# Kernel optimization log

Measured on AMD Instinct MI355X. Metric: run time of the kernel, lower is better.

Reference implementation:

```python
import jax, jax.numpy as jnp
import numpy as np

DIM = 1024
HEADS = 16
HEAD_DIM = DIM // HEADS
SCALE = HEAD_DIM ** -0.5


def setup_inputs() -> dict:
    key = jax.random.key(0)
    k1, k2, k3, k4 = jax.random.split(key, 4)
    x = jax.random.normal(k1, (8, 1024, DIM), dtype=jnp.float32)
    # qkv: Linear(dim, 3*dim), bias=False; proj: Linear(dim, dim) with bias
    w_qkv = jax.random.normal(k2, (DIM, 3 * DIM), dtype=jnp.float32) * (DIM ** -0.5)
    w_proj = jax.random.normal(k3, (DIM, DIM), dtype=jnp.float32) * (DIM ** -0.5)
    b_proj = jax.random.normal(k4, (DIM,), dtype=jnp.float32) * 0.02
    return {"x": x, "w_qkv": w_qkv, "w_proj": w_proj, "b_proj": b_proj}


def reference(x, w_qkv, w_proj, b_proj):
    b, n, dim = x.shape
    h, d = HEADS, HEAD_DIM
    qkv = x @ w_qkv                                  # [b, n, 3*dim]
    qkv = qkv.reshape(b, n, 3, h, d)                  # split (qkv h d)
    q = jnp.transpose(qkv[:, :, 0], (0, 2, 1, 3))     # [b, h, n, d]
    k = jnp.transpose(qkv[:, :, 1], (0, 2, 1, 3))
    v = jnp.transpose(qkv[:, :, 2], (0, 2, 1, 3))
    dots = jnp.einsum('bhid,bhjd->bhij', q, k) * SCALE
    attn = jax.nn.softmax(dots, axis=-1)              # [b, h, n, n]
    out = jnp.einsum('bhij,bhjd->bhid', attn, v)      # [b, h, n, d]
    out = jnp.transpose(out, (0, 2, 1, 3)).reshape(b, n, dim)
    return out @ w_proj + b_proj
```

## Files before the change

kernel.cpp:

```cpp
#include <hip/hip_runtime.h>
#include <hip/hip_bf16.h>
#include <stdint.h>


typedef __attribute__((ext_vector_type(8))) short  short8;
typedef __attribute__((ext_vector_type(4))) float  floatx4;

#define MFMA_BF16(a, b, c) __builtin_amdgcn_mfma_f32_16x16x32_bf16((a), (b), (c), 0, 0, 0)

__device__ __forceinline__ uint16_t f2b(float f) {
    uint32_t i; __builtin_memcpy(&i, &f, 4);
    uint32_t r = i + 0x7FFFu + ((i >> 16) & 1u);
    return (uint16_t)(r >> 16);
}

#if defined(__has_builtin)
#if __has_builtin(__builtin_amdgcn_cvt_pk_bf16_f32)
#define HAVE_PK_BF16 1
#endif
#if __has_builtin(__builtin_amdgcn_exp2f)
#define EXP2F __builtin_amdgcn_exp2f
#endif
#endif
#ifndef EXP2F
#define EXP2F exp2f
#endif

__device__ __forceinline__ uint32_t pk_bf16(float a, float b) {
#ifdef HAVE_PK_BF16
    typedef __attribute__((ext_vector_type(2))) __bf16 bf16x2;
    bf16x2 v = __builtin_amdgcn_cvt_pk_bf16_f32(a, b);
    uint32_t u; __builtin_memcpy(&u, &v, 4); return u;
#else
    return (uint32_t)f2b(a) | ((uint32_t)f2b(b) << 16);
#endif
}

__device__ __forceinline__ void p32swap(uint32_t& a, uint32_t& b) {
    asm("v_permlane32_swap_b32 %0, %1" : "+v"(a), "+v"(b));
}
__device__ __forceinline__ void p16swap(uint32_t& a, uint32_t& b) {
    asm("v_permlane16_swap_b32 %0, %1" : "+v"(a), "+v"(b));
}

__device__ __forceinline__ void async16(uint16_t* lds, const uint16_t* g) {
    __builtin_amdgcn_global_load_lds(
        (const __attribute__((address_space(1))) uint32_t*)g,
        (__attribute__((address_space(3))) uint32_t*)lds,
        16, 0, 0);
}

__global__ __launch_bounds__(256) void cvt_f32_bf16(
    const float* __restrict__ in, uint16_t* __restrict__ out, int n4)
{
    const int i = blockIdx.x * 256 + threadIdx.x;
    if (i < n4) {
        const float4 v = ((const float4*)in)[i];
        ushort4 o;
        o.x = f2b(v.x); o.y = f2b(v.y); o.z = f2b(v.z); o.w = f2b(v.w);
        ((ushort4*)out)[i] = o;
    }
}

__global__ __launch_bounds__(256) void transpose_k(
    const float* __restrict__ in, uint16_t* __restrict__ out, int R, int C)
{
    __shared__ uint16_t t[32][33];
    const int bx = blockIdx.x * 32;
    const int by = blockIdx.y * 32;
    const int tx = threadIdx.x & 31, ty = threadIdx.x >> 5;
    #pragma unroll
    for (int j = 0; j < 32; j += 8)
        t[ty + j][tx] = f2b(in[(size_t)(by + ty + j) * C + bx + tx]);
    __syncthreads();
    #pragma unroll
    for (int j = 0; j < 32; j += 8)
        out[(size_t)(bx + ty + j) * R + by + tx] = t[tx][ty + j];
}

template <int EPI>
__global__ __launch_bounds__(256, 2) void gemm_bt(
    const uint16_t* __restrict__ A, const uint16_t* __restrict__ Bt,
    uint16_t* __restrict__ C, float* __restrict__ Cf,
    const float* __restrict__ bias, int M, int N, int K)
{
    __shared__ uint16_t As[128 * 64];
    __shared__ uint16_t Bs[128 * 64];

    const int tid  = threadIdx.x;
    const int lane = tid & 63, quad = lane >> 4, l16 = lane & 15;
    const int wv   = tid >> 6;
    const int wm   = (wv >> 1) * 64, wn = (wv & 1) * 64;

    const int lid = blockIdx.y * gridDim.x + blockIdx.x;
    const int nxl = gridDim.x >> 3;
    const int xcd = lid & 7, loc = lid >> 3;
    const int bx  = xcd * nxl + (loc % nxl);
    const int by  = loc / nxl;
    const int tm  = by * 128, tn = bx * 128;

    floatx4 acc[4][4] = {};

    for (int kt = 0; kt < K; kt += 64) {
        __syncthreads();
        #pragma unroll
        for (int i = 0; i < 4; i++) {
            const int li  = i * 256 + tid;
            const int row = li >> 3;
            const int cg  = (li & 7) ^ (row & 7);
            async16(&As[li * 8], &A[(size_t)(tm + row) * K + kt + cg * 8]);
        }
        #pragma unroll
        for (int i = 0; i < 4; i++) {
            const int li  = i * 256 + tid;
            const int row = li >> 3;
            const int cg  = (li & 7) ^ (row & 7);
            async16(&Bs[li * 8], &Bt[(size_t)(tn + row) * K + kt + cg * 8]);
        }
        __syncthreads();
        #pragma unroll
        for (int kc = 0; kc < 2; kc++) {
            short8 af[4], bf[4];
            #pragma unroll
            for (int mb = 0; mb < 4; mb++) {
                const int row = wm + mb * 16 + l16;
                const int g   = kc * 4 + quad;
                af[mb] = *(const short8*)&As[row * 64 + ((g ^ (row & 7)) * 8)];
            }
            #pragma unroll
            for (int nb = 0; nb < 4; nb++) {
                const int row = wn + nb * 16 + l16;
                const int g   = kc * 4 + quad;
                bf[nb] = *(const short8*)&Bs[row * 64 + ((g ^ (row & 7)) * 8)];
            }
            #pragma unroll
            for (int mb = 0; mb < 4; mb++)
                #pragma unroll
                for (int nb = 0; nb < 4; nb++)
                    acc[mb][nb] = MFMA_BF16(af[mb], bf[nb], acc[mb][nb]);
        }
    }

    if (EPI == 0) {
        const int which = (tn + wn) >> 10;
        if (which == 2) {
            #pragma unroll
            for (int nb = 0; nb < 4; nb++) {
                const int col = tn + wn + nb * 16 + l16;
                const int hh = (col >> 6) & 15, dd = col & 63;
                #pragma unroll
                for (int mb = 0; mb < 4; mb++) {
                    const int gm = tm + wm + mb * 16 + quad * 4;
                    const int b  = gm >> 10, n = gm & 1023;
                    const size_t rgn = (size_t)(256 + b * 16 + hh) * 65536;
                    uint2 o;
                    o.x = pk_bf16(acc[mb][nb][0], acc[mb][nb][1]);
                    o.y = pk_bf16(acc[mb][nb][2], acc[mb][nb][3]);
                    *(uint2*)&C[rgn + (size_t)dd * 1024 + n] = o;
                }
            }
        } else {
            const float qs = (which == 0) ? 0.18033688011112043f : 1.0f;
            #pragma unroll
            for (int nb = 0; nb < 4; nb++) {
                const int col = tn + wn + nb * 16 + l16;
                const int hh = (col >> 6) & 15, dd = col & 63;
                #pragma unroll
                for (int mb = 0; mb < 4; mb++)
                    #pragma unroll
                    for (int r = 0; r < 4; r++) {
                        const int gm = tm + wm + mb * 16 + quad * 4 + r;
                        const int b  = gm >> 10, n = gm & 1023;
                        const size_t rgn = (size_t)(which * 128 + b * 16 + hh) * 65536;
                        C[rgn + (size_t)n * 64 + dd] = f2b(acc[mb][nb][r] * qs);
                    }
            }
        }
    } else {
        #pragma unroll
        for (int nb = 0; nb < 4; nb++) {
            const int col = tn + wn + nb * 16 + l16;
            const float bv = bias[col];
            #pragma unroll
            for (int mb = 0; mb < 4; mb++)
                #pragma unroll
                for (int r = 0; r < 4; r++) {
                    const int gm = tm + wm + mb * 16 + quad * 4 + r;
                    Cf[(size_t)gm * N + col] = acc[mb][nb][r] + bv;
                }
        }
    }
}

__global__ __launch_bounds__(256, 4) void attn_fa(
    const uint16_t* __restrict__ qkv, uint16_t* __restrict__ out)
{
    __shared__ uint16_t Ks[128 * 64];
    __shared__ uint16_t Vs[64 * 128];

    const int tid  = threadIdx.x;
    const int lane = tid & 63, quad = lane >> 4, l16 = lane & 15;
    const int wv   = tid >> 6;
    const int bh   = blockIdx.y;
    const int q0   = blockIdx.x * 128 + wv * 32;

    const size_t qbase  = (size_t)bh * 65536;
    const size_t kbase  = (size_t)(128 + bh) * 65536;
    const size_t vtbase = (size_t)(256 + bh) * 65536;

    short8 qf[2][2];
    #pragma unroll
    for (int nq = 0; nq < 2; nq++)
        #pragma unroll
        for (int ks = 0; ks < 2; ks++)
            qf[nq][ks] = *(const short8*)&qkv[qbase + (size_t)(q0 + nq * 16 + l16) * 64 + ks * 32 + quad * 8];

    floatx4 Oacc[2][4] = {};
    float lpart[2] = {0.f, 0.f};

    for (int kb = 0; kb < 8; kb++) {
        __syncthreads();
        #pragma unroll
        for (int i = 0; i < 4; i++) {
            const int li  = i * 256 + tid;
            const int row = li >> 3;
            const int cg  = (li & 7) ^ (row & 7);
            async16(&Ks[li * 8], &qkv[kbase + (size_t)(kb * 128 + row) * 64 + cg * 8]);
        }
        #pragma unroll
        for (int i = 0; i < 4; i++) {
            const int li  = i * 256 + tid;
            const int row = li >> 4;
            const int cg  = (li & 15) ^ (row & 15);
            async16(&Vs[li * 8], &qkv[vtbase + (size_t)row * 1024 + kb * 128 + cg * 8]);
        }
        __syncthreads();

        #pragma unroll
        for (int h = 0; h < 2; h++) {
            short8 pf[2][2];
            #pragma unroll
            for (int kk = 0; kk < 2; kk++) {
                floatx4 st[2][2];
                #pragma unroll
                for (int mb2 = 0; mb2 < 2; mb2++) {
                    const int krow = h * 64 + (kk * 2 + mb2) * 16 + l16;
                    const int g0 = quad, g1 = 4 + quad;
                    short8 kf0 = *(const short8*)&Ks[krow * 64 + ((g0 ^ (krow & 7)) * 8)];
                    short8 kf1 = *(const short8*)&Ks[krow * 64 + ((g1 ^ (krow & 7)) * 8)];
                    #pragma unroll
                    for (int nq = 0; nq < 2; nq++) {
                        floatx4 z = {};
                        z = MFMA_BF16(kf0, qf[nq][0], z);
                        z = MFMA_BF16(kf1, qf[nq][1], z);
                        st[mb2][nq] = z;
                    }
                }
                #pragma unroll
                for (int mb2 = 0; mb2 < 2; mb2++)
                    #pragma unroll
                    for (int nq = 0; nq < 2; nq++)
                        #pragma unroll
                        for (int r = 0; r < 4; r++) {
                            const float p = EXP2F(st[mb2][nq][r]);
                            st[mb2][nq][r] = p;
                            lpart[nq] += p;
                        }
                #pragma unroll
                for (int nq = 0; nq < 2; nq++) {
                    uint32_t w0 = pk_bf16(st[0][nq][0], st[0][nq][1]);
                    uint32_t w1 = pk_bf16(st[0][nq][2], st[0][nq][3]);
                    uint32_t w2 = pk_bf16(st[1][nq][0], st[1][nq][1]);
                    uint32_t w3 = pk_bf16(st[1][nq][2], st[1][nq][3]);
                    p32swap(w0, w2); p16swap(w0, w2);
                    p32swap(w1, w3); p16swap(w1, w3);
                    uint32_t w[4] = { w0, w1, w2, w3 };
                    __builtin_memcpy(&pf[nq][kk], w, 16);
                }
            }
            #pragma unroll
            for (int nb = 0; nb < 4; nb++)
                #pragma unroll
                for (int kk = 0; kk < 2; kk++) {
                    const int vrow = nb * 16 + l16;
                    const int g    = h * 8 + kk * 4 + quad;
                    short8 vf = *(const short8*)&Vs[vrow * 128 + ((g ^ (vrow & 15)) * 8)];
                    #pragma unroll
                    for (int qb = 0; qb < 2; qb++)
                        Oacc[qb][nb] = MFMA_BF16(pf[qb][kk], vf, Oacc[qb][nb]);
                }
        }
    }

    float linv[2];
    #pragma unroll
    for (int nq = 0; nq < 2; nq++) {
        float l = lpart[nq];
        l += __shfl_xor(l, 16);
        l += __shfl_xor(l, 32);
        linv[nq] = 1.f / l;
    }
    float inv[2][4];
    #pragma unroll
    for (int qb = 0; qb < 2; qb++)
        #pragma unroll
        for (int r = 0; r < 4; r++)
            inv[qb][r] = __shfl(linv[qb], quad * 4 + r);

    const int b = bh >> 4, hh = bh & 15;
    #pragma unroll
    for (int qb = 0; qb < 2; qb++)
        #pragma unroll
        for (int nb = 0; nb < 4; nb++)
            #pragma unroll
            for (int r = 0; r < 4; r++) {
                const int n = q0 + qb * 16 + quad * 4 + r;
                out[((size_t)(b * 1024 + n)) * 1024 + hh * 64 + nb * 16 + l16] =
                    f2b(Oacc[qb][nb][r] * inv[qb][r]);
            }
}

extern "C" void kernel_launch(void* const* d_in, const int* in_sizes, int n_in,
                              void* d_out, int out_size, void* d_ws, size_t ws_size,
                              hipStream_t stream)
{
    const float* x      = (const float*)d_in[0];
    const float* w_qkv  = (const float*)d_in[1];
    const float* w_proj = (const float*)d_in[2];
    const float* b_proj = (const float*)d_in[3];
    float* out = (float*)d_out;

    uint16_t* ws   = (uint16_t*)d_ws;
    uint16_t* xb   = ws;
    uint16_t* wTq  = xb  + 8192 * 1024;
    uint16_t* wTp  = wTq + 3072 * 1024;
    uint16_t* qkvb = wTp + 1024 * 1024;
    uint16_t* ao   = xb;

    cvt_f32_bf16<<<8192, 256, 0, stream>>>(x, xb, 8192 * 1024 / 4);
    transpose_k<<<dim3(96, 32), 256, 0, stream>>>(w_qkv, wTq, 1024, 3072);
    transpose_k<<<dim3(32, 32), 256, 0, stream>>>(w_proj, wTp, 1024, 1024);
    gemm_bt<0><<<dim3(24, 64), 256, 0, stream>>>(xb, wTq, qkvb, nullptr, nullptr, 8192, 3072, 1024);
    attn_fa<<<dim3(8, 128), 256, 0, stream>>>(qkvb, ao);
    gemm_bt<1><<<dim3(8, 64), 256, 0, stream>>>(ao, wTp, nullptr, out, b_proj, 8192, 1024, 1024);
}
```

Before: 237.5 us.

## Double-buffer GEMM LDS tiles with 256x128 blocks and split-phase prefetch

Rewrites the bf16 GEMM main loop to use 512-thread blocks covering 256x128 output tiles with double-buffered LDS. Global-to-LDS async loads for the next k-tile are issued in halves between the two MFMA phases, with explicit vmcnt waits, barriers and setprio, so memory traffic overlaps compute instead of stalling at each k-step. This doubles LDS use to about 96KB per block and relies on the epilogue still mapping wm/wn correctly with the larger M tile. Grid sizes are halved in M to match.

New measurement: 245.8 us. 3.5% more time.

```diff
diff --git a/kernel.cpp b/kernel.cpp
--- a/kernel.cpp
+++ b/kernel.cpp
@@ -78,66 +78,120 @@
         out[(size_t)(bx + ty + j) * R + by + tx] = t[tx][ty + j];
 }
 
+__device__ __forceinline__ void stage_a(uint16_t* dst, const uint16_t* src,
+                                        int row0, int K, int kt, int half, int tid)
+{
+    #pragma unroll
+    for (int s = 0; s < 2; s++) {
+        const int li = s * 512 + tid;
+        const int r  = li >> 3;
+        const int R  = ((r >> 5) << 6) + half * 32 + (r & 31);
+        const int cg = (li & 7) ^ (R & 7);
+        async16(&dst[R * 64 + (li & 7) * 8],
+                &src[(size_t)(row0 + R) * K + kt + cg * 8]);
+    }
+}
+__device__ __forceinline__ void stage_b(uint16_t* dst, const uint16_t* src,
+                                        int row0, int K, int kt, int tid)
+{
+    #pragma unroll
+    for (int s = 0; s < 2; s++) {
+        const int li = s * 512 + tid;
+        const int r  = li >> 3;
+        const int cg = (li & 7) ^ (r & 7);
+        async16(&dst[li * 8],
+                &src[(size_t)(row0 + r) * K + kt + cg * 8]);
+    }
+}
+
 template <int EPI>
-__global__ __launch_bounds__(256, 2) void gemm_bt(
+__global__ __launch_bounds__(512, 2) void gemm_bt(
     const uint16_t* __restrict__ A, const uint16_t* __restrict__ Bt,
     uint16_t* __restrict__ C, float* __restrict__ Cf,
     const float* __restrict__ bias, int M, int N, int K)
 {
-    __shared__ uint16_t As[128 * 64];
-    __shared__ uint16_t Bs[128 * 64];
+    __shared__ uint16_t As[2][256 * 64];
+    __shared__ uint16_t Bs[2][128 * 64];
 
     const int tid  = threadIdx.x;
     const int lane = tid & 63, quad = lane >> 4, l16 = lane & 15;
     const int wv   = tid >> 6;
-    const int wm   = (wv >> 1) * 64, wn = (wv & 1) * 64;
+    const int wm   = (wv >> 1) * 64;
+    const int wn   = (wv & 1) * 64;
 
     const int lid = blockIdx.y * gridDim.x + blockIdx.x;
     const int nxl = gridDim.x >> 3;
     const int xcd = lid & 7, loc = lid >> 3;
     const int bx  = xcd * nxl + (loc % nxl);
     const int by  = loc / nxl;
-    const int tm  = by * 128, tn = bx * 128;
+    const int tm  = by * 256, tn = bx * 128;
+
+    const int nt = K >> 6;
 
     floatx4 acc[4][4] = {};
 
-    for (int kt = 0; kt < K; kt += 64) {
-        __syncthreads();
-        #pragma unroll
-        for (int i = 0; i < 4; i++) {
-            const int li  = i * 256 + tid;
-            const int row = li >> 3;
-            const int cg  = (li & 7) ^ (row & 7);
-            async16(&As[li * 8], &A[(size_t)(tm + row) * K + kt + cg * 8]);
-        }
-        #pragma unroll
-        for (int i = 0; i < 4; i++) {
-            const int li  = i * 256 + tid;
-            const int row = li >> 3;
-            const int cg  = (li & 7) ^ (row & 7);
-            async16(&Bs[li * 8], &Bt[(size_t)(tn + row) * K + kt + cg * 8]);
-        }
-        __syncthreads();
-        #pragma unroll
-        for (int kc = 0; kc < 2; kc++) {
-            short8 af[4], bf[4];
-            #pragma unroll
-            for (int mb = 0; mb < 4; mb++) {
-                const int row = wm + mb * 16 + l16;
-                const int g   = kc * 4 + quad;
-                af[mb] = *(const short8*)&As[row * 64 + ((g ^ (row & 7)) * 8)];
+    stage_a(&As[0][0], A,  tm, K, 0,  0, tid);
+    stage_a(&As[0][0], A,  tm, K, 0,  1, tid);
+    stage_b(&Bs[0][0], Bt, tn, K, 0,     tid);
+    stage_a(&As[1][0], A,  tm, K, 64, 0, tid);
+    __builtin_amdgcn_sched_barrier(0);
+    asm volatile("s_waitcnt vmcnt(2)" ::: "memory");
+    __builtin_amdgcn_s_barrier();
+
+    for (int t = 0; t < nt; t++) {
+        const int cur = t & 1;
+        const uint16_t* Ac = &As[cur][0];
+        const uint16_t* Bc = &Bs[cur][0];
+        #pragma unroll
+        for (int p = 0; p < 2; p++) {
+            short8 af[2][2], bfr[4][2];
+            #pragma unroll
+            for (int mb = 0; mb < 2; mb++) {
+                const int row = wm + p * 32 + mb * 16 + l16;
+                #pragma unroll
+                for (int kc = 0; kc < 2; kc++) {
+                    const int g = kc * 4 + quad;
+                    af[mb][kc] = *(const short8*)&Ac[row * 64 + ((g ^ (row & 7)) * 8)];
+                }
             }
             #pragma unroll
             for (int nb = 0; nb < 4; nb++) {
                 const int row = wn + nb * 16 + l16;
-                const int g   = kc * 4 + quad;
-                bf[nb] = *(const short8*)&Bs[row * 64 + ((g ^ (row & 7)) * 8)];
-            }
-            #pragma unroll
-            for (int mb = 0; mb < 4; mb++)
+                #pragma unroll
+                for (int kc = 0; kc < 2; kc++) {
+                    const int g = kc * 4 + quad;
+                    bfr[nb][kc] = *(const short8*)&Bc[row * 64 + ((g ^ (row & 7)) * 8)];
+                }
+            }
+            if (p == 0) {
+                if (t + 1 < nt) {
+                    stage_b(&Bs[cur ^ 1][0], Bt, tn, K, (t + 1) << 6, tid);
+                    stage_a(&As[cur ^ 1][0], A,  tm, K, (t + 1) << 6, 1, tid);
+                }
+            } else {
+                if (t + 2 < nt)
+                    stage_a(&As[cur][0], A, tm, K, (t + 2) << 6, 0, tid);
+            }
+            __builtin_amdgcn_sched_barrier(0);
+            __builtin_amdgcn_s_barrier();
+            asm volatile("" ::: "memory");
+            __builtin_amdgcn_s_setprio(1);
+            #pragma unroll
+            for (int mb = 0; mb < 2; mb++)
                 #pragma unroll
                 for (int nb = 0; nb < 4; nb++)
-                    acc[mb][nb] = MFMA_BF16(af[mb], bf[nb], acc[mb][nb]);
+                    #pragma unroll
+                    for (int kc = 0; kc < 2; kc++)
+                        acc[p * 2 + mb][nb] =
+                            MFMA_BF16(af[mb][kc], bfr[nb][kc], acc[p * 2 + mb][nb]);
+            __builtin_amdgcn_s_setprio(0);
+            __builtin_amdgcn_sched_barrier(0);
+            if (p == 1) {
+                if (t + 2 < nt) { asm volatile("s_waitcnt vmcnt(2)" ::: "memory"); }
+                else            { asm volatile("s_waitcnt vmcnt(0)" ::: "memory"); }
+            }
+            __builtin_amdgcn_s_barrier();
+            __builtin_amdgcn_sched_barrier(0);
         }
     }
 
@@ -340,7 +394,7 @@
     cvt_f32_bf16<<<8192, 256, 0, stream>>>(x, xb, 8192 * 1024 / 4);
     transpose_k<<<dim3(96, 32), 256, 0, stream>>>(w_qkv, wTq, 1024, 3072);
     transpose_k<<<dim3(32, 32), 256, 0, stream>>>(w_proj, wTp, 1024, 1024);
-    gemm_bt<0><<<dim3(24, 64), 256, 0, stream>>>(xb, wTq, qkvb, nullptr, nullptr, 8192, 3072, 1024);
+    gemm_bt<0><<<dim3(24, 32), 512, 0, stream>>>(xb, wTq, qkvb, nullptr, nullptr, 8192, 3072, 1024);
     attn_fa<<<dim3(8, 128), 256, 0, stream>>>(qkvb, ao);
-    gemm_bt<1><<<dim3(8, 64), 256, 0, stream>>>(ao, wTp, nullptr, out, b_proj, 8192, 1024, 1024);
-}
+    gemm_bt<1><<<dim3(8, 32), 512, 0, stream>>>(ao, wTp, nullptr, out, b_proj, 8192, 1024, 1024);
+}
```

## Double-buffer K/V tiles in attention with async prefetch two blocks ahead

Applied to the files above, without the earlier changes.

Replaces the single 128-key K/V shared tile, loaded synchronously each iteration, with two 64-key buffers. The loads for block kb+2 are issued right after block kb is consumed, and manual vmcnt waits plus barriers keep global loads overlapped with MFMA and exp compute. The aim is to hide global-to-LDS latency that the old load-then-sync pattern exposed. In exchange it relies on hand-counted vmcnt values, adds more barriers per key because tiles are smaller, and drops the V swizzle from 16-way to 8-way.

Result: faster. 232.4 us (-2.1%).

```diff
diff --git a/kernel.cpp b/kernel.cpp
--- a/kernel.cpp
+++ b/kernel.cpp
@@ -195,8 +195,8 @@
 __global__ __launch_bounds__(256, 4) void attn_fa(
     const uint16_t* __restrict__ qkv, uint16_t* __restrict__ out)
 {
-    __shared__ uint16_t Ks[128 * 64];
-    __shared__ uint16_t Vs[64 * 128];
+    __shared__ uint16_t Ks[2][64 * 64];
+    __shared__ uint16_t Vs[2][64 * 64];
 
     const int tid  = threadIdx.x;
     const int lane = tid & 63, quad = lane >> 4, l16 = lane & 15;
@@ -214,82 +214,118 @@
         #pragma unroll
         for (int ks = 0; ks < 2; ks++)
             qf[nq][ks] = *(const short8*)&qkv[qbase + (size_t)(q0 + nq * 16 + l16) * 64 + ks * 32 + quad * 8];
+    asm volatile("s_waitcnt vmcnt(0)" ::: "memory");
+
+    const int sr  = tid >> 3;
+    const int sc  = tid & 7;
 
     floatx4 Oacc[2][4] = {};
     float lpart[2] = {0.f, 0.f};
 
-    for (int kb = 0; kb < 8; kb++) {
-        __syncthreads();
-        #pragma unroll
-        for (int i = 0; i < 4; i++) {
-            const int li  = i * 256 + tid;
+    #pragma unroll
+    for (int pb = 0; pb < 2; pb++) {
+        #pragma unroll
+        for (int s = 0; s < 2; s++) {
+            const int li  = s * 256 + tid;
             const int row = li >> 3;
             const int cg  = (li & 7) ^ (row & 7);
-            async16(&Ks[li * 8], &qkv[kbase + (size_t)(kb * 128 + row) * 64 + cg * 8]);
-        }
-        #pragma unroll
-        for (int i = 0; i < 4; i++) {
-            const int li  = i * 256 + tid;
-            const int row = li >> 4;
-            const int cg  = (li & 15) ^ (row & 15);
-            async16(&Vs[li * 8], &qkv[vtbase + (size_t)row * 1024 + kb * 128 + cg * 8]);
-        }
-        __syncthreads();
-
-        #pragma unroll
-        for (int h = 0; h < 2; h++) {
-            short8 pf[2][2];
+            async16(&Ks[pb][li * 8], &qkv[kbase + (size_t)(pb * 64 + row) * 64 + cg * 8]);
+        }
+        #pragma unroll
+        for (int s = 0; s < 2; s++) {
+            const int li  = s * 256 + tid;
+            const int row = li >> 3;
+            const int cg  = (li & 7) ^ (row & 7);
+            async16(&Vs[pb][li * 8], &qkv[vtbase + (size_t)row * 1024 + pb * 64 + cg * 8]);
+        }
+    }
+    __builtin_amdgcn_sched_barrier(0);
+    asm volatile("s_waitcnt vmcnt(4)" ::: "memory");
+    __builtin_amdgcn_s_barrier();
+
+    for (int kb = 0; kb < 16; kb++) {
+        const uint16_t* Kc = &Ks[kb & 1][0];
+        const uint16_t* Vc = &Vs[kb & 1][0];
+
+        short8 pf[2][2];
+        #pragma unroll
+        for (int kk = 0; kk < 2; kk++) {
+            floatx4 st[2][2];
+            #pragma unroll
+            for (int mb2 = 0; mb2 < 2; mb2++) {
+                const int krow = (kk * 2 + mb2) * 16 + l16;
+                short8 kf0 = *(const short8*)&Kc[krow * 64 + ((quad ^ (krow & 7)) * 8)];
+                short8 kf1 = *(const short8*)&Kc[krow * 64 + (((4 + quad) ^ (krow & 7)) * 8)];
+                #pragma unroll
+                for (int nq = 0; nq < 2; nq++) {
+                    floatx4 z = {};
+                    z = MFMA_BF16(kf0, qf[nq][0], z);
+                    z = MFMA_BF16(kf1, qf[nq][1], z);
+                    st[mb2][nq] = z;
+                }
+            }
+            #pragma unroll
+            for (int mb2 = 0; mb2 < 2; mb2++)
+                #pragma unroll
+                for (int nq = 0; nq < 2; nq++)
+                    #pragma unroll
+                    for (int r = 0; r < 4; r++) {
+                        const float p = EXP2F(st[mb2][nq][r]);
+                        st[mb2][nq][r] = p;
+                        lpart[nq] += p;
+                    }
+            #pragma unroll
+            for (int nq = 0; nq < 2; nq++) {
+                uint32_t w0 = pk_bf16(st[0][nq][0], st[0][nq][1]);
+                uint32_t w1 = pk_bf16(st[0][nq][2], st[0][nq][3]);
+                uint32_t w2 = pk_bf16(st[1][nq][0], st[1][nq][1]);
+                uint32_t w3 = pk_bf16(st[1][nq][2], st[1][nq][3]);
+                p32swap(w0, w2); p16swap(w0, w2);
+                p32swap(w1, w3); p16swap(w1, w3);
+                uint32_t w[4] = { w0, w1, w2, w3 };
+                __builtin_memcpy(&pf[nq][kk], w, 16);
+            }
+        }
+        #pragma unroll
+        for (int nb = 0; nb < 4; nb++)
             #pragma unroll
             for (int kk = 0; kk < 2; kk++) {
-                floatx4 st[2][2];
-                #pragma unroll
-                for (int mb2 = 0; mb2 < 2; mb2++) {
-                    const int krow = h * 64 + (kk * 2 + mb2) * 16 + l16;
-                    const int g0 = quad, g1 = 4 + quad;
-                    short8 kf0 = *(const short8*)&Ks[krow * 64 + ((g0 ^ (krow & 7)) * 8)];
-                    short8 kf1 = *(const short8*)&Ks[krow * 64 + ((g1 ^ (krow & 7)) * 8)];
-                    #pragma unroll
-                    for (int nq = 0; nq < 2; nq++) {
-                        floatx4 z = {};
-                        z = MFMA_BF16(kf0, qf[nq][0], z);
-                        z = MFMA_BF16(kf1, qf[nq][1], z);
-                        st[mb2][nq] = z;
-                    }
-                }
-                #pragma unroll
-                for (int mb2 = 0; mb2 < 2; mb2++)
-                    #pragma unroll
-                    for (int nq = 0; nq < 2; nq++)
-                        #pragma unroll
-                        for (int r = 0; r < 4; r++) {
-                            const float p = EXP2F(st[mb2][nq][r]);
-                            st[mb2][nq][r] = p;
-                            lpart[nq] += p;
-                        }
-                #pragma unroll
-                for (int nq = 0; nq < 2; nq++) {
-                    uint32_t w0 = pk_bf16(st[0][nq][0], st[0][nq][1]);
-                    uint32_t w1 = pk_bf16(st[0][nq][2], st[0][nq][3]);
-                    uint32_t w2 = pk_bf16(st[1][nq][0], st[1][nq][1]);
-                    uint32_t w3 = pk_bf16(st[1][nq][2], st[1][nq][3]);
-                    p32swap(w0, w2); p16swap(w0, w2);
-                    p32swap(w1, w3); p16swap(w1, w3);
-                    uint32_t w[4] = { w0, w1, w2, w3 };
-                    __builtin_memcpy(&pf[nq][kk], w, 16);
-                }
-            }
-            #pragma unroll
-            for (int nb = 0; nb < 4; nb++)
-                #pragma unroll
-                for (int kk = 0; kk < 2; kk++) {
-                    const int vrow = nb * 16 + l16;
-                    const int g    = h * 8 + kk * 4 + quad;
-                    short8 vf = *(const short8*)&Vs[vrow * 128 + ((g ^ (vrow & 15)) * 8)];
-                    #pragma unroll
-                    for (int qb = 0; qb < 2; qb++)
-                        Oacc[qb][nb] = MFMA_BF16(pf[qb][kk], vf, Oacc[qb][nb]);
-                }
-        }
+                const int vrow = nb * 16 + l16;
+                const int g    = kk * 4 + quad;
+                short8 vf = *(const short8*)&Vc[vrow * 64 + ((g ^ (vrow & 7)) * 8)];
+                #pragma unroll
+                for (int qb = 0; qb < 2; qb++)
+                    Oacc[qb][nb] = MFMA_BF16(pf[qb][kk], vf, Oacc[qb][nb]);
+            }
+
+        __builtin_amdgcn_sched_barrier(0);
+        __builtin_amdgcn_s_barrier();
+        if (kb + 2 < 16) {
+            uint16_t* Kd = &Ks[kb & 1][0];
+            uint16_t* Vd = &Vs[kb & 1][0];
+            const int kn = kb + 2;
+            #pragma unroll
+            for (int s = 0; s < 2; s++) {
+                const int li  = s * 256 + tid;
+                const int row = li >> 3;
+                const int cg  = (li & 7) ^ (row & 7);
+                async16(&Kd[li * 8], &qkv[kbase + (size_t)(kn * 64 + row) * 64 + cg * 8]);
+            }
+            #pragma unroll
+            for (int s = 0; s < 2; s++) {
+                const int li  = s * 256 + tid;
+                const int row = li >> 3;
+                const int cg  = (li & 7) ^ (row & 7);
+                async16(&Vd[li * 8], &qkv[vtbase + (size_t)row * 1024 + kn * 64 + cg * 8]);
+            }
+            __builtin_amdgcn_sched_barrier(0);
+            asm volatile("s_waitcnt vmcnt(4)" ::: "memory");
+        } else {
+            __builtin_amdgcn_sched_barrier(0);
+            asm volatile("s_waitcnt vmcnt(0)" ::: "memory");
+        }
+        __builtin_amdgcn_s_barrier();
+        __builtin_amdgcn_sched_barrier(0);
     }
 
     float linv[2];
```
